# Performance work log

Hardware: AMD Instinct MI355X
Metric: run time of the kernel (lower is better)

## Reference

```python
import jax, jax.numpy as jnp
import numpy as np

B, S, D, E = 4, 2048, 512, 32

def setup_inputs() -> dict:
    key = jax.random.key(0)
    k1, k2, k3 = jax.random.split(key, 3)
    x = jax.random.normal(k1, (B, S, D), dtype=jnp.float32)
    # glorot-ish scaling for weights
    gate_w = jax.random.normal(k2, (D, E), dtype=jnp.float32) * (1.0 / np.sqrt(D))
    gate_b = jnp.zeros((E,), dtype=jnp.float32)
    expert_w = jax.random.normal(k3, (E, D, D), dtype=jnp.float32) * (1.0 / np.sqrt(D))
    return {"x": x, "gate_w": gate_w, "gate_b": gate_b, "expert_w": expert_w}

def reference(x, gate_w, gate_b, expert_w):
    # gate_scores: [B,S,E] (context=None -> route on x itself)
    gate = jax.nn.softmax(jnp.einsum('bsd,de->bse', x, gate_w) + gate_b, axis=-1)
    # Dense soft-MoE: sum_e gate[b,s,e] * (x[b,s,:] @ expert_w[e])
    # Single einsum avoids materializing the [B,S,E,D] intermediate.
    out = jnp.einsum('bse,bsd,edf->bsf', gate, x, expert_w)
    return out
```

## Files before the change

kernel.cpp:

```cpp
#include <hip/hip_runtime.h>

#define TOK 8192
#define DIM 512
#define NE  32
#define KTOT (NE * DIM)

#define BM 128
#define BN 128
#define BK 64

typedef float f32x4 __attribute__((ext_vector_type(4)));
typedef short s16x8 __attribute__((ext_vector_type(8)));

typedef const void __attribute__((address_space(1)))* gp1_t;
typedef void __attribute__((address_space(3)))* lp3_t;

__device__ __forceinline__ void gl_lds16(const void* g, void* l) {
    __builtin_amdgcn_global_load_lds((gp1_t)g, (lp3_t)l, 16, 0, 0);
}

__device__ __forceinline__ ushort f2bf(float f) {
    unsigned u = __builtin_bit_cast(unsigned, f);
    unsigned r = (u + 0x7fffu + ((u >> 16) & 1u)) >> 16;
    return (ushort)r;
}

__global__ __launch_bounds__(256) void k_cvt_wt(const float* __restrict__ w,
                                                ushort* __restrict__ wt) {
    __shared__ float tile[32][33];
    const int e = blockIdx.z;
    const int f0 = blockIdx.x * 32;
    const int d0 = blockIdx.y * 32;
    const int tx = threadIdx.x, ty = threadIdx.y;
    const float* we = w + (size_t)e * DIM * DIM;
#pragma unroll
    for (int i = ty; i < 32; i += 8)
        tile[i][tx] = we[(size_t)(d0 + i) * DIM + f0 + tx];
    __syncthreads();
#pragma unroll
    for (int i = ty; i < 32; i += 8)
        wt[(size_t)(f0 + i) * KTOT + e * DIM + d0 + tx] = f2bf(tile[tx][i]);
}

__global__ __launch_bounds__(256) void k_gates(const float* __restrict__ x,
                                               const float* __restrict__ gw,
                                               const float* __restrict__ gb,
                                               float* __restrict__ G,
                                               ushort* __restrict__ xb) {
    __shared__ float xs[DIM];
    __shared__ float part[256];
    __shared__ float logits[NE];
    const int t = blockIdx.x;
    const int tid = threadIdx.x;
    float v0 = x[(size_t)t * DIM + tid];
    float v1 = x[(size_t)t * DIM + tid + 256];
    xs[tid] = v0;
    xs[tid + 256] = v1;
    xb[(size_t)t * DIM + tid] = f2bf(v0);
    xb[(size_t)t * DIM + tid + 256] = f2bf(v1);
    __syncthreads();
    const int e = tid & 31;
    const int ch = tid >> 5;
    float s = 0.f;
#pragma unroll 8
    for (int i = 0; i < 64; ++i) {
        int d = ch * 64 + i;
        s += xs[d] * gw[d * NE + e];
    }
    part[tid] = s;
    __syncthreads();
    if (tid < NE) {
        float l = gb[tid];
#pragma unroll
        for (int c = 0; c < 8; ++c) l += part[c * 32 + tid];
        logits[tid] = l;
    }
    __syncthreads();
    float ex = 0.f;
    if (tid < NE) {
        float mx = -1e30f;
#pragma unroll
        for (int o = 0; o < NE; ++o) mx = fmaxf(mx, logits[o]);
        ex = expf(logits[tid] - mx);
        part[tid] = ex;
    }
    __syncthreads();
    if (tid < NE) {
        float sum = 0.f;
#pragma unroll
        for (int o = 0; o < NE; ++o) sum += part[o];
        G[(size_t)t * NE + tid] = ex / sum;
    }
}

__global__ __launch_bounds__(512, 2) void k_moe_gemm(const ushort* __restrict__ xb,
                                                     const ushort* __restrict__ wt,
                                                     const float* __restrict__ G,
                                                     float* __restrict__ out0,
                                                     float* __restrict__ out1) {
    __shared__ __align__(16) ushort As[BM * BK];
    __shared__ __align__(16) ushort Bs[BN * BK];
    __shared__ float Gs[BM][17];

    const int tid = threadIdx.x;
    const int m0 = blockIdx.y * BM;
    const int n0 = blockIdx.x * BN;
    const int e0 = blockIdx.z * 16;
    float* __restrict__ dst = blockIdx.z ? out1 : out0;

    for (int i = tid; i < BM * 16; i += 512) {
        int r = i >> 4, c = i & 15;
        Gs[r][c] = G[(size_t)(m0 + r) * NE + e0 + c];
    }

    const int lane = tid & 63;
    const int wave = tid >> 6;
    const int wm = (wave & 3) * 32;
    const int wn = (wave >> 2) * 64;
    const int l15 = lane & 15;
    const int q = lane >> 4;
    const int keyR = l15 & 7;

    const f32x4 zv = {0.f, 0.f, 0.f, 0.f};
    f32x4 acc[2][4];
#pragma unroll
    for (int i = 0; i < 2; ++i)
#pragma unroll
        for (int j = 0; j < 4; ++j) acc[i][j] = zv;

    const int srow = tid >> 3;
    const int chunk = tid & 7;
    const int scol = ((chunk ^ (srow & 7)) * 8);
    const ushort* aBase = xb + (size_t)(m0 + srow) * DIM + scol;
    const ushort* bBase = wt + (size_t)(n0 + srow) * KTOT + scol;
    char* aLds = (char*)As + tid * 16;
    char* bLds = (char*)Bs + tid * 16;

#pragma unroll 1
    for (int ee = 0; ee < 16; ++ee) {
        const int e = e0 + ee;
        f32x4 pacc[2][4];
#pragma unroll
        for (int i = 0; i < 2; ++i)
#pragma unroll
            for (int j = 0; j < 4; ++j) pacc[i][j] = zv;

#pragma unroll 1
        for (int kt = 0; kt < 8; ++kt) {
            const int kd = kt * BK;
            const ushort* aS = aBase + kd;
            const ushort* bS = bBase + (size_t)e * DIM + kd;
            gl_lds16(aS, aLds);
            gl_lds16(aS + (size_t)64 * DIM, aLds + 8192);
            gl_lds16(bS, bLds);
            gl_lds16(bS + (size_t)64 * KTOT, bLds + 8192);
            __syncthreads();
#pragma unroll
            for (int ks = 0; ks < 2; ++ks) {
                const int swz = ((ks * 4 + q) ^ keyR) * 16;
                s16x8 a[2], b[4];
#pragma unroll
                for (int i = 0; i < 2; ++i)
                    a[i] = *(const s16x8*)((const char*)As +
                           (wm + i * 16 + l15) * (BK * 2) + swz);
#pragma unroll
                for (int j = 0; j < 4; ++j)
                    b[j] = *(const s16x8*)((const char*)Bs +
                           (wn + j * 16 + l15) * (BK * 2) + swz);
#pragma unroll
                for (int i = 0; i < 2; ++i)
#pragma unroll
                    for (int j = 0; j < 4; ++j)
                        pacc[i][j] = __builtin_amdgcn_mfma_f32_16x16x32_bf16(
                            a[i], b[j], pacc[i][j], 0, 0, 0);
            }
            __syncthreads();
        }

#pragma unroll
        for (int i = 0; i < 2; ++i) {
            const int tl = wm + i * 16 + q * 4;
            const float g0 = Gs[tl + 0][ee];
            const float g1 = Gs[tl + 1][ee];
            const float g2 = Gs[tl + 2][ee];
            const float g3 = Gs[tl + 3][ee];
#pragma unroll
            for (int j = 0; j < 4; ++j) {
                acc[i][j][0] += g0 * pacc[i][j][0];
                acc[i][j][1] += g1 * pacc[i][j][1];
                acc[i][j][2] += g2 * pacc[i][j][2];
                acc[i][j][3] += g3 * pacc[i][j][3];
            }
        }
    }

#pragma unroll
    for (int i = 0; i < 2; ++i) {
        const int tl = m0 + wm + i * 16 + q * 4;
#pragma unroll
        for (int j = 0; j < 4; ++j) {
            const int f = n0 + wn + j * 16 + l15;
            float* p = dst + (size_t)tl * DIM + f;
            p[0 * DIM] = acc[i][j][0];
            p[1 * DIM] = acc[i][j][1];
            p[2 * DIM] = acc[i][j][2];
            p[3 * DIM] = acc[i][j][3];
        }
    }
}

__global__ __launch_bounds__(256) void k_reduce(float* __restrict__ out,
                                                const float* __restrict__ P) {
    int i = (blockIdx.x * 256 + threadIdx.x) * 4;
    float4 a = *(const float4*)(out + i);
    float4 b = *(const float4*)(P + i);
    a.x += b.x; a.y += b.y; a.z += b.z; a.w += b.w;
    *(float4*)(out + i) = a;
}

extern "C" void kernel_launch(void* const* d_in, const int* in_sizes, int n_in,
                              void* d_out, int out_size, void* d_ws, size_t ws_size,
                              hipStream_t stream) {
    const float* x  = (const float*)d_in[0];
    const float* gw = (const float*)d_in[1];
    const float* gb = (const float*)d_in[2];
    const float* w  = (const float*)d_in[3];
    float* out = (float*)d_out;

    char* ws = (char*)d_ws;
    ushort* xb = (ushort*)ws;
    ushort* wt = (ushort*)(ws + (8u << 20));
    float*  G  = (float*)(ws + (24u << 20));
    float*  P  = (float*)(ws + (25u << 20));

    k_cvt_wt<<<dim3(16, 16, NE), dim3(32, 8, 1), 0, stream>>>(w, wt);
    k_gates<<<dim3(TOK), dim3(256), 0, stream>>>(x, gw, gb, G, xb);
    k_moe_gemm<<<dim3(DIM / BN, TOK / BM, 2), dim3(512), 0, stream>>>(xb, wt, G, out, P);
    k_reduce<<<dim3(TOK * DIM / (256 * 4)), dim3(256), 0, stream>>>(out, P);
}
```

Measured before the change: 257.8 us.

## Add 4-way expert split GEMM with per-step gate scaling, rework gates and transpose

Adds a new MoE GEMM with 256 threads, 64x64 warp tiles and a 4-way expert split. It applies the gate weight right after each k-step's MFMA pair rather than keeping a per-expert partial accumulator. The gates kernel now processes 8 tokens per block using float4 loads and warp-shuffle softmax, the weight transpose uses 64x64 tiles, and the final reduce sums three partial buffers. This aims to raise occupancy and cut launch and gate overhead. In exchange it needs more workspace, adds partial-output memory traffic, and rounds to the accumulator more often.

```diff
diff --git a/kernel.cpp b/kernel.cpp
--- a/kernel.cpp
+++ b/kernel.cpp
@@ -27,18 +27,18 @@
 
 __global__ __launch_bounds__(256) void k_cvt_wt(const float* __restrict__ w,
                                                 ushort* __restrict__ wt) {
-    __shared__ float tile[32][33];
+    __shared__ float tile[64][65];
     const int e = blockIdx.z;
-    const int f0 = blockIdx.x * 32;
-    const int d0 = blockIdx.y * 32;
-    const int tx = threadIdx.x, ty = threadIdx.y;
+    const int f0 = blockIdx.x * 64;
+    const int d0 = blockIdx.y * 64;
+    const int tx = threadIdx.x & 63, ty = threadIdx.x >> 6;
     const float* we = w + (size_t)e * DIM * DIM;
 #pragma unroll
-    for (int i = ty; i < 32; i += 8)
+    for (int i = ty; i < 64; i += 4)
         tile[i][tx] = we[(size_t)(d0 + i) * DIM + f0 + tx];
     __syncthreads();
 #pragma unroll
-    for (int i = ty; i < 32; i += 8)
+    for (int i = ty; i < 64; i += 4)
         wt[(size_t)(f0 + i) * KTOT + e * DIM + d0 + tx] = f2bf(tile[tx][i]);
 }
 
@@ -47,49 +47,154 @@
                                                const float* __restrict__ gb,
                                                float* __restrict__ G,
                                                ushort* __restrict__ xb) {
-    __shared__ float xs[DIM];
-    __shared__ float part[256];
-    __shared__ float logits[NE];
-    const int t = blockIdx.x;
+    __shared__ float xs[8 * DIM];
+    const int t0 = blockIdx.x * 8;
     const int tid = threadIdx.x;
-    float v0 = x[(size_t)t * DIM + tid];
-    float v1 = x[(size_t)t * DIM + tid + 256];
-    xs[tid] = v0;
-    xs[tid + 256] = v1;
-    xb[(size_t)t * DIM + tid] = f2bf(v0);
-    xb[(size_t)t * DIM + tid + 256] = f2bf(v1);
+    const float* xBase = x + (size_t)t0 * DIM;
+#pragma unroll
+    for (int k = 0; k < 4; ++k) {
+        int i4 = (k * 256 + tid) * 4;
+        float4 v = *(const float4*)(xBase + i4);
+        xs[i4 + 0] = v.x; xs[i4 + 1] = v.y; xs[i4 + 2] = v.z; xs[i4 + 3] = v.w;
+        ushort4 o;
+        o.x = f2bf(v.x); o.y = f2bf(v.y); o.z = f2bf(v.z); o.w = f2bf(v.w);
+        *(ushort4*)(xb + (size_t)t0 * DIM + i4) = o;
+    }
     __syncthreads();
+    const int tok = tid >> 5;
     const int e = tid & 31;
-    const int ch = tid >> 5;
-    float s = 0.f;
+    float l = gb[e];
+    const float* xr = xs + tok * DIM;
 #pragma unroll 8
-    for (int i = 0; i < 64; ++i) {
-        int d = ch * 64 + i;
-        s += xs[d] * gw[d * NE + e];
-    }
-    part[tid] = s;
+    for (int d = 0; d < DIM; ++d)
+        l += xr[d] * gw[d * NE + e];
+    float mx = l;
+#pragma unroll
+    for (int m = 16; m >= 1; m >>= 1) mx = fmaxf(mx, __shfl_xor(mx, m));
+    float ex = expf(l - mx);
+    float s = ex;
+#pragma unroll
+    for (int m = 16; m >= 1; m >>= 1) s += __shfl_xor(s, m);
+    G[(size_t)(t0 + tok) * NE + e] = ex / s;
+}
+
+__global__ __launch_bounds__(256, 3) void k_moe_gemm4(const ushort* __restrict__ xb,
+                                                      const ushort* __restrict__ wt,
+                                                      const float* __restrict__ G,
+                                                      float* __restrict__ out,
+                                                      float* __restrict__ P1,
+                                                      float* __restrict__ P2,
+                                                      float* __restrict__ P3) {
+    __shared__ __align__(16) ushort As[BM * BK];
+    __shared__ __align__(16) ushort Bs[BN * BK];
+    __shared__ float Gs[8][BM];
+
+    const int tid = threadIdx.x;
+    const int m0 = blockIdx.y * BM;
+    const int n0 = blockIdx.x * BN;
+    const int z = blockIdx.z;
+    const int e0 = z * 8;
+    float* __restrict__ dst = (z == 0) ? out : (z == 1) ? P1 : (z == 2) ? P2 : P3;
+
+    for (int i = tid; i < 8 * BM; i += 256) {
+        int e = i & 7, r = i >> 3;
+        Gs[e][r] = G[(size_t)(m0 + r) * NE + e0 + e];
+    }
+
+    const int lane = tid & 63;
+    const int wave = tid >> 6;
+    const int wm = (wave & 1) * 64;
+    const int wn = (wave >> 1) * 64;
+    const int l15 = lane & 15;
+    const int q = lane >> 4;
+    const int keyR = l15 & 7;
+
+    const int swz0 = ((0 * 4 + q) ^ keyR) * 16;
+    const int swz1 = ((1 * 4 + q) ^ keyR) * 16;
+    int ra[4][2], rb[4][2];
+#pragma unroll
+    for (int i = 0; i < 4; ++i) {
+        ra[i][0] = (wm + i * 16 + l15) * 128 + swz0;
+        ra[i][1] = (wm + i * 16 + l15) * 128 + swz1;
+        rb[i][0] = (wn + i * 16 + l15) * 128 + swz0;
+        rb[i][1] = (wn + i * 16 + l15) * 128 + swz1;
+    }
+
+    const f32x4 zv = {0.f, 0.f, 0.f, 0.f};
+    f32x4 acc[4][4];
+#pragma unroll
+    for (int i = 0; i < 4; ++i)
+#pragma unroll
+        for (int j = 0; j < 4; ++j) acc[i][j] = zv;
+
+    const int srow = tid >> 3;
+    const int chunk = tid & 7;
+    const int scol = ((chunk ^ (srow & 7)) * 8);
+    const ushort* aBase = xb + (size_t)(m0 + srow) * DIM + scol;
+    const ushort* bBase = wt + (size_t)(n0 + srow) * KTOT + scol;
+    char* aLds = (char*)As + tid * 16;
+    char* bLds = (char*)Bs + tid * 16;
+
     __syncthreads();
-    if (tid < NE) {
-        float l = gb[tid];
-#pragma unroll
-        for (int c = 0; c < 8; ++c) l += part[c * 32 + tid];
-        logits[tid] = l;
-    }
-    __syncthreads();
-    float ex = 0.f;
-    if (tid < NE) {
-        float mx = -1e30f;
-#pragma unroll
-        for (int o = 0; o < NE; ++o) mx = fmaxf(mx, logits[o]);
-        ex = expf(logits[tid] - mx);
-        part[tid] = ex;
-    }
-    __syncthreads();
-    if (tid < NE) {
-        float sum = 0.f;
-#pragma unroll
-        for (int o = 0; o < NE; ++o) sum += part[o];
-        G[(size_t)t * NE + tid] = ex / sum;
+
+#pragma unroll 1
+    for (int ee = 0; ee < 8; ++ee) {
+        const int e = e0 + ee;
+        f32x4 gt[4];
+#pragma unroll
+        for (int i = 0; i < 4; ++i)
+            gt[i] = *(const f32x4*)&Gs[ee][wm + i * 16 + q * 4];
+
+#pragma unroll 1
+        for (int kt = 0; kt < 8; ++kt) {
+            const int kd = kt * BK;
+            const ushort* aS = aBase + kd;
+            const ushort* bS = bBase + (size_t)e * DIM + kd;
+#pragma unroll
+            for (int r = 0; r < 4; ++r) {
+                gl_lds16(aS + (size_t)r * 32 * DIM, aLds + r * 4096);
+                gl_lds16(bS + (size_t)r * 32 * KTOT, bLds + r * 4096);
+            }
+            __syncthreads();
+
+            s16x8 a[4][2];
+#pragma unroll
+            for (int i = 0; i < 4; ++i) {
+                a[i][0] = *(const s16x8*)((const char*)As + ra[i][0]);
+                a[i][1] = *(const s16x8*)((const char*)As + ra[i][1]);
+            }
+#pragma unroll
+            for (int j = 0; j < 4; ++j) {
+                s16x8 b0 = *(const s16x8*)((const char*)Bs + rb[j][0]);
+                s16x8 b1 = *(const s16x8*)((const char*)Bs + rb[j][1]);
+#pragma unroll
+                for (int i = 0; i < 4; ++i) {
+                    f32x4 p = __builtin_amdgcn_mfma_f32_16x16x32_bf16(
+                        a[i][0], b0, zv, 0, 0, 0);
+                    p = __builtin_amdgcn_mfma_f32_16x16x32_bf16(
+                        a[i][1], b1, p, 0, 0, 0);
+                    acc[i][j][0] += gt[i][0] * p[0];
+                    acc[i][j][1] += gt[i][1] * p[1];
+                    acc[i][j][2] += gt[i][2] * p[2];
+                    acc[i][j][3] += gt[i][3] * p[3];
+                }
+            }
+            __syncthreads();
+        }
+    }
+
+#pragma unroll
+    for (int i = 0; i < 4; ++i) {
+        const int tl = m0 + wm + i * 16 + q * 4;
+#pragma unroll
+        for (int j = 0; j < 4; ++j) {
+            const int f = n0 + wn + j * 16 + l15;
+            float* p = dst + (size_t)tl * DIM + f;
+            p[0 * DIM] = acc[i][j][0];
+            p[1 * DIM] = acc[i][j][1];
+            p[2 * DIM] = acc[i][j][2];
+            p[3 * DIM] = acc[i][j][3];
+        }
     }
 }
 
@@ -210,11 +315,19 @@
 }
 
 __global__ __launch_bounds__(256) void k_reduce(float* __restrict__ out,
-                                                const float* __restrict__ P) {
+                                                const float* __restrict__ P1,
+                                                const float* __restrict__ P2,
+                                                const float* __restrict__ P3,
+                                                int nP) {
     int i = (blockIdx.x * 256 + threadIdx.x) * 4;
     float4 a = *(const float4*)(out + i);
-    float4 b = *(const float4*)(P + i);
+    float4 b = *(const float4*)(P1 + i);
     a.x += b.x; a.y += b.y; a.z += b.z; a.w += b.w;
+    if (nP == 3) {
+        float4 c = *(const float4*)(P2 + i);
+        float4 d = *(const float4*)(P3 + i);
+        a.x += c.x + d.x; a.y += c.y + d.y; a.z += c.z + d.z; a.w += c.w + d.w;
+    }
     *(float4*)(out + i) = a;
 }
 
@@ -231,10 +344,20 @@
     ushort* xb = (ushort*)ws;
     ushort* wt = (ushort*)(ws + (8u << 20));
     float*  G  = (float*)(ws + (24u << 20));
-    float*  P  = (float*)(ws + (25u << 20));
-
-    k_cvt_wt<<<dim3(16, 16, NE), dim3(32, 8, 1), 0, stream>>>(w, wt);
-    k_gates<<<dim3(TOK), dim3(256), 0, stream>>>(x, gw, gb, G, xb);
-    k_moe_gemm<<<dim3(DIM / BN, TOK / BM, 2), dim3(512), 0, stream>>>(xb, wt, G, out, P);
-    k_reduce<<<dim3(TOK * DIM / (256 * 4)), dim3(256), 0, stream>>>(out, P);
-}
+    float*  P1 = (float*)(ws + (25u << 20));
+    float*  P2 = (float*)(ws + (41u << 20));
+    float*  P3 = (float*)(ws + (57u << 20));
+
+    k_cvt_wt<<<dim3(8, 8, NE), dim3(256), 0, stream>>>(w, wt);
+    k_gates<<<dim3(TOK / 8), dim3(256), 0, stream>>>(x, gw, gb, G, xb);
+
+    if (ws_size >= ((size_t)73u << 20)) {
+        k_moe_gemm4<<<dim3(DIM / BN, TOK / BM, 4), dim3(256), 0, stream>>>(
+            xb, wt, G, out, P1, P2, P3);
+        k_reduce<<<dim3(TOK * DIM / 1024), dim3(256), 0, stream>>>(out, P1, P2, P3, 3);
+    } else {
+        k_moe_gemm<<<dim3(DIM / BN, TOK / BM, 2), dim3(512), 0, stream>>>(
+            xb, wt, G, out, P1);
+        k_reduce<<<dim3(TOK * DIM / 1024), dim3(256), 0, stream>>>(out, P1, P1, P1, 1);
+    }
+}
```

Measured after the change: 311.5 us. 1.21x slower.
